# Kernel optimization log

Measured on AMD Instinct MI355X. Metric: run time of the kernel, lower is better.

Reference implementation:

```python
import jax, jax.numpy as jnp
import numpy as np

NUM_EXPERTS = 4


def _conv1x1(w, b, x):
    # w: [out,in], b: [out], x: [B,in,H,W]
    return jnp.einsum('oc,bchw->bohw', w, x) + b[None, :, None, None]


def _sobel(x):
    c = x.shape[1]
    kx = jnp.array([[-1., 0., 1.], [-2., 0., 2.], [-1., 0., 1.]], dtype=x.dtype)
    ky = jnp.array([[-1., -2., -1.], [0., 0., 0.], [1., 2., 1.]], dtype=x.dtype)
    wx = jnp.broadcast_to(kx[None, None], (c, 1, 3, 3))
    wy = jnp.broadcast_to(ky[None, None], (c, 1, 3, 3))
    dn = ('NCHW', 'OIHW', 'NCHW')
    gx = jax.lax.conv_general_dilated(x, wx, (1, 1), [(1, 1), (1, 1)],
                                      dimension_numbers=dn, feature_group_count=c)
    gy = jax.lax.conv_general_dilated(x, wy, (1, 1), [(1, 1), (1, 1)],
                                      dimension_numbers=dn, feature_group_count=c)
    return gx, gy


def _bilinear_sample(x, gx, gy):
    # torch F.grid_sample(mode='bilinear', padding_mode='zeros', align_corners=False)
    # x: [B,C,H,W]; gx, gy: [B,Hs,Ws] normalized coords in [-1,1]
    B, C, H, W = x.shape
    ix = ((gx + 1.0) * W - 1.0) * 0.5
    iy = ((gy + 1.0) * H - 1.0) * 0.5
    x0 = jnp.floor(ix)
    y0 = jnp.floor(iy)
    wx1 = ix - x0
    wx0 = 1.0 - wx1
    wy1 = iy - y0
    wy0 = 1.0 - wy1
    xf = x.reshape(B, C, H * W)

    def gather(xc, yc):
        valid = (xc >= 0) & (xc <= W - 1) & (yc >= 0) & (yc <= H - 1)
        xi = jnp.clip(xc, 0, W - 1).astype(jnp.int32)
        yi = jnp.clip(yc, 0, H - 1).astype(jnp.int32)
        idx = yi * W + xi  # [B,Hs,Ws]
        v = jax.vmap(lambda xb, ib: xb[:, ib])(xf, idx)  # [B,C,Hs,Ws]
        return v * valid[:, None].astype(x.dtype)

    return (gather(x0, y0) * (wx0 * wy0)[:, None]
            + gather(x0 + 1, y0) * (wx1 * wy0)[:, None]
            + gather(x0, y0 + 1) * (wx0 * wy1)[:, None]
            + gather(x0 + 1, y0 + 1) * (wx1 * wy1)[:, None])


def _forward(x, wc_e, we_e, wb1, bb1, wb2, bb2, wr, br, wo, bo, wcv, bcv, scale, scale2):
    B, c, h, w = x.shape
    sh = round(h * scale)
    sw = round(w * scale2)

    grad_x, grad_y = _sobel(x)

    # relative-offset coordinate embedding, [1,4,sh,sw]
    ih = (jnp.arange(sh, dtype=x.dtype) + 0.5) / scale
    coor_h = ih - jnp.floor(ih + 0.001) - 0.5  # [sh]
    iw = (jnp.arange(sw, dtype=x.dtype) + 0.5) / scale2
    coor_w = iw - jnp.floor(iw + 0.001) - 0.5  # [sw]
    inp = jnp.stack([
        jnp.full((sh, sw), 1.0 / scale2, dtype=x.dtype),
        jnp.full((sh, sw), 1.0 / scale, dtype=x.dtype),
        jnp.broadcast_to(coor_h[:, None], (sh, sw)),
        jnp.broadcast_to(coor_w[None, :], (sh, sw)),
    ], axis=0)[None]

    emb = jax.nn.relu(_conv1x1(wb2, bb2, jax.nn.relu(_conv1x1(wb1, bb1, inp))))
    offset = _conv1x1(wo, bo, emb)                 # [1,2,sh,sw]
    routing = jax.nn.sigmoid(_conv1x1(wr, br, emb))  # [1,E,sh,sw]

    # per-pixel soft mixture of expert compress/expand matrices
    rw = routing.reshape(NUM_EXPERTS, sh * sw).T   # [N,E]
    wc = (rw @ wc_e.reshape(NUM_EXPERTS, -1)).reshape(sh, sw, c // 8, c)
    we = (rw @ we_e.reshape(NUM_EXPERTS, -1)).reshape(sh, sw, c, c // 8)

    feat = _conv1x1(wcv, bcv, jnp.concatenate([x, grad_x, grad_y], axis=1))  # [B,64,h,w]

    # base grid (align_corners=True-style normalization, as in the source) + learned offsets
    gx0 = ((jnp.arange(sw, dtype=x.dtype) + 0.5) / scale2 - 0.5) * 2.0 / (w - 1) - 1.0
    gy0 = ((jnp.arange(sh, dtype=x.dtype) + 0.5) / scale - 0.5) * 2.0 / (h - 1) - 1.0
    gx = jnp.broadcast_to(gx0[None, None, :] + offset[:, 0] * (2.0 / (w - 1)), (B, sh, sw))
    gy = jnp.broadcast_to(gy0[None, :, None] + offset[:, 1] * (2.0 / (h - 1)), (B, sh, sw))

    fea0 = _bilinear_sample(feat, gx, gy)          # [B,64,sh,sw]

    mid = jnp.einsum('hwkc,bchw->bhwk', wc, fea0)  # per-pixel compress (k=C//8)
    out = jnp.einsum('hwck,bhwk->bchw', we, mid)   # per-pixel expand
    return out + fea0


def setup_inputs() -> dict:
    key = jax.random.key(0)
    ks = jax.random.split(key, 13)
    s = 0.05
    return {
        'x': jax.random.normal(ks[0], (2, 64, 192, 192), jnp.float32),
        'weight_compress': jax.random.normal(ks[1], (4, 8, 64), jnp.float32) * s,
        'weight_expand': jax.random.normal(ks[2], (4, 64, 8), jnp.float32) * s,
        'w_body1': jax.random.normal(ks[3], (64, 4), jnp.float32) * s,
        'b_body1': jax.random.normal(ks[4], (64,), jnp.float32) * s,
        'w_body2': jax.random.normal(ks[5], (64, 64), jnp.float32) * s,
        'b_body2': jax.random.normal(ks[6], (64,), jnp.float32) * s,
        'w_routing': jax.random.normal(ks[7], (4, 64), jnp.float32) * s,
        'b_routing': jax.random.normal(ks[8], (4,), jnp.float32) * s,
        'w_offset': jax.random.normal(ks[9], (2, 64), jnp.float32) * s,
        'b_offset': jax.random.normal(ks[10], (2,), jnp.float32) * s,
        'w_conv': jax.random.normal(ks[11], (64, 192), jnp.float32) * s,
        'b_conv': jax.random.normal(ks[12], (64,), jnp.float32) * s,
        'scale': 2,
        'scale2': 2,
    }


def reference(x, weight_compress, weight_expand, w_body1, b_body1, w_body2, b_body2,
              w_routing, b_routing, w_offset, b_offset, w_conv, b_conv, scale, scale2):
    return _forward(x, weight_compress, weight_expand, w_body1, b_body1, w_body2, b_body2,
                    w_routing, b_routing, w_offset, b_offset, w_conv, b_conv, scale, scale2)
```

## Files before the change

kernel.cpp:

```cpp
#include <hip/hip_runtime.h>
#include <hip/hip_bf16.h>
#include <math.h>

#define BN  2
#define CN  64
#define HN  192
#define WN  192
#define SH  384
#define SW  384
#define HW  (HN * WN)
#define NPIX (BN * HN * WN)

typedef __attribute__((ext_vector_type(8))) short bf16x8;
typedef __attribute__((ext_vector_type(4))) float f32x4;

#define KPAD 200

__device__ inline unsigned short f2bf(float f) {
    unsigned int u = __float_as_uint(f);
    u += 0x7fffu + ((u >> 16) & 1u);
    return (unsigned short)(u >> 16);
}

__device__ inline void sobel_col(const float* __restrict__ xc,
    size_t oT, size_t oM, size_t oB, int j, int jL, int jR,
    float mt, float mb, float mLt, float mLm, float mLb,
    float mRt, float mRm, float mRb, bool isL, bool isR,
    float& m_out, float& sx, float& sy)
{
    float t   = xc[oT + j] * mt;
    float m   = xc[oM + j];
    float btm = xc[oB + j] * mb;
    float hLt = xc[oT + jL] * mLt;
    float hLm = xc[oM + jL] * mLm;
    float hLb = xc[oB + jL] * mLb;
    float hRt = xc[oT + jR] * mRt;
    float hRm = xc[oM + jR] * mRm;
    float hRb = xc[oB + jR] * mRb;
    float tl  = __shfl_up(t, 1),   ml_ = __shfl_up(m, 1),   bl_ = __shfl_up(btm, 1);
    float tr  = __shfl_down(t, 1), mr_ = __shfl_down(m, 1), br_ = __shfl_down(btm, 1);
    float n0 = isL ? hLt : tl;
    float n3 = isL ? hLm : ml_;
    float n6 = isL ? hLb : bl_;
    float n2 = isR ? hRt : tr;
    float n5 = isR ? hRm : mr_;
    float n8 = isR ? hRb : br_;
    m_out = m;
    sx = (n2 - n0) + 2.f * (n5 - n3) + (n8 - n6);
    sy = (n6 - n0) + 2.f * (btm - t) + (n8 - n2);
}

__global__ __launch_bounds__(256) void feat_kernel(
    const float* __restrict__ x,
    const float* __restrict__ wcv,
    const float* __restrict__ bcv,
    float* __restrict__ feat)
{
    __shared__ unsigned short Bs[64 * KPAD];

    int bi = blockIdx.x;
    int jt = bi % 3;
    int t2 = bi / 3;
    int i  = t2 % HN;
    int b  = t2 / HN;
    int j0 = jt * 64;

    int tid  = threadIdx.x;
    int w    = __builtin_amdgcn_readfirstlane(tid >> 6);
    int lane = tid & 63;

    int mrow = (w << 4) + (lane & 15);
    int kb   = (lane >> 4) << 3;
    bf16x8 afrag[6];
    {
        const float* wr_ = wcv + mrow * 192 + kb;
#pragma unroll
        for (int ks = 0; ks < 6; ++ks) {
            float4 lo = *(const float4*)(wr_ + ks * 32);
            float4 hi = *(const float4*)(wr_ + ks * 32 + 4);
            bf16x8 a;
            a[0] = (short)f2bf(lo.x); a[1] = (short)f2bf(lo.y);
            a[2] = (short)f2bf(lo.z); a[3] = (short)f2bf(lo.w);
            a[4] = (short)f2bf(hi.x); a[5] = (short)f2bf(hi.y);
            a[6] = (short)f2bf(hi.z); a[7] = (short)f2bf(hi.w);
            afrag[ks] = a;
        }
    }

    bool ok_t = (i > 0), ok_b = (i < HN - 1);
    bool okL = (j0 > 0), okR = (j0 + 64 < WN);
    float mt = ok_t ? 1.f : 0.f, mb = ok_b ? 1.f : 0.f;
    int rT = ok_t ? i - 1 : i;
    int rB = ok_b ? i + 1 : i;
    int jL = okL ? j0 - 1 : j0;
    int jR = okR ? j0 + 64 : j0;
    float mLt = okL ? mt : 0.f, mLm = okL ? 1.f : 0.f, mLb = okL ? mb : 0.f;
    float mRt = okR ? mt : 0.f, mRm = okR ? 1.f : 0.f, mRb = okR ? mb : 0.f;
    bool isL = (lane == 0), isR = (lane == 63);

    const float* xb = x + (size_t)b * CN * HW;
    size_t oT = (size_t)rT * WN, oM = (size_t)i * WN, oB = (size_t)rB * WN;
    int j = j0 + lane;

    unsigned short* brow = Bs + lane * KPAD;
#pragma unroll 2
    for (int cp = 0; cp < 8; ++cp) {
        int c0 = (w << 4) + (cp << 1);
        float m0, sx0, sy0, m1, sx1, sy1;
        sobel_col(xb + (size_t)c0 * HW, oT, oM, oB, j, jL, jR,
                  mt, mb, mLt, mLm, mLb, mRt, mRm, mRb, isL, isR, m0, sx0, sy0);
        sobel_col(xb + (size_t)(c0 + 1) * HW, oT, oM, oB, j, jL, jR,
                  mt, mb, mLt, mLm, mLb, mRt, mRm, mRb, isL, isR, m1, sx1, sy1);
        *(unsigned int*)(brow + c0)       = (unsigned int)f2bf(m0)  | ((unsigned int)f2bf(m1)  << 16);
        *(unsigned int*)(brow + 64 + c0)  = (unsigned int)f2bf(sx0) | ((unsigned int)f2bf(sx1) << 16);
        *(unsigned int*)(brow + 128 + c0) = (unsigned int)f2bf(sy0) | ((unsigned int)f2bf(sy1) << 16);
    }

    __syncthreads();

    f32x4 acc[4] = {};
    const unsigned short* bp = Bs + (lane & 15) * KPAD + ((lane >> 4) << 3);
#pragma unroll
    for (int nt = 0; nt < 4; ++nt) {
        const unsigned short* bnt = bp + nt * 16 * KPAD;
#pragma unroll
        for (int ks = 0; ks < 6; ++ks) {
            bf16x8 bf = *(const bf16x8*)(bnt + ks * 32);
            acc[nt] = __builtin_amdgcn_mfma_f32_16x16x32_bf16(afrag[ks], bf, acc[nt], 0, 0, 0);
        }
    }

    int n0 = j0 + (lane & 15);
    int mbase = (w << 4) + ((lane >> 4) << 2);
    size_t outb = (size_t)b * CN * HW + (size_t)i * WN;
#pragma unroll
    for (int rr = 0; rr < 4; ++rr) {
        int m = mbase + rr;
        float bias = bcv[m];
        size_t rowb = outb + (size_t)m * HW + n0;
#pragma unroll
        for (int nt = 0; nt < 4; ++nt)
            feat[rowb + nt * 16] = acc[nt][rr] + bias;
    }
}

__device__ inline void run_mlp(int lane, float in0, float in1, float chv, float cwv,
    const float* __restrict__ wb1, const float* __restrict__ bb1,
    const float* __restrict__ wb2, const float* __restrict__ bb2,
    const float* __restrict__ wr,  const float* __restrict__ wo, float p[6])
{
    float4 w1 = ((const float4*)wb1)[lane];
    float h1 = fmaxf(bb1[lane] + w1.x * in0 + w1.y * in1 + w1.z * chv + w1.w * cwv, 0.f);
    const float4* w2row = (const float4*)(wb2 + lane * 64);
    float acc = bb2[lane];
#pragma unroll
    for (int q = 0; q < 16; ++q) {
        float4 wv = w2row[q];
        acc += wv.x * __shfl(h1, q * 4 + 0)
             + wv.y * __shfl(h1, q * 4 + 1)
             + wv.z * __shfl(h1, q * 4 + 2)
             + wv.w * __shfl(h1, q * 4 + 3);
    }
    float h2 = fmaxf(acc, 0.f);
#pragma unroll
    for (int e = 0; e < 4; ++e) p[e] = wr[e * 64 + lane] * h2;
#pragma unroll
    for (int e = 0; e < 2; ++e) p[4 + e] = wo[e * 64 + lane] * h2;
#pragma unroll
    for (int m = 1; m < 64; m <<= 1) {
#pragma unroll
        for (int e = 0; e < 6; ++e) p[e] += __shfl_xor(p[e], m);
    }
}

__global__ __launch_bounds__(256) void mlp_table_kernel(
    const float* __restrict__ wb1, const float* __restrict__ bb1,
    const float* __restrict__ wb2, const float* __restrict__ bb2,
    const float* __restrict__ wr,  const float* __restrict__ br,
    const float* __restrict__ wo,  const float* __restrict__ bo,
    const float* __restrict__ wce, const float* __restrict__ wee,
    const int* __restrict__ scale_p, const int* __restrict__ scale2_p,
    float* __restrict__ tblEntry, unsigned short* __restrict__ tblM)
{
    __shared__ float reL[8];
    __shared__ float wcmL[2 * 512];
    __shared__ float wemL[2 * 512];

    int sc = scale_p[0], sc2 = scale2_p[0];
    int tid = threadIdx.x;
    int lane = tid & 63;
    float scale = (float)sc, scale2 = (float)sc2;
    float in0 = 1.f / scale2, in1 = 1.f / scale;
    bool fast = (sc2 == 2 && sc <= 16);

    if (fast) {
        int pi = blockIdx.x;
        if (pi >= sc) return;
        if (tid < 64) {
            float ih = (pi + 0.5f) / scale;
            float chv = ih - floorf(ih + 0.001f) - 0.5f;
            float p0[6], p1[6];
            {
                float iw = 0.5f / scale2;
                float cwv = iw - floorf(iw + 0.001f) - 0.5f;
                run_mlp(lane, in0, in1, chv, cwv, wb1, bb1, wb2, bb2, wr, wo, p0);
            }
            {
                float iw = 1.5f / scale2;
                float cwv = iw - floorf(iw + 0.001f) - 0.5f;
                run_mlp(lane, in0, in1, chv, cwv, wb1, bb1, wb2, bb2, wr, wo, p1);
            }
            if (lane == 0) {
                float* t0 = tblEntry + (pi * 2 + 0) * 8;
                float* t1 = tblEntry + (pi * 2 + 1) * 8;
#pragma unroll
                for (int e = 0; e < 4; ++e) {
                    float rE = 1.f / (1.f + expf(-(p0[e] + br[e])));
                    float rO = 1.f / (1.f + expf(-(p1[e] + br[e])));
                    t0[e] = rE; t1[e] = rO;
                    reL[e] = rE; reL[4 + e] = rO;
                }
                t0[4] = p0[4] + bo[0]; t0[5] = p0[5] + bo[1];
                t1[4] = p1[4] + bo[0]; t1[5] = p1[5] + bo[1];
            }
        }
        __syncthreads();
        float reE0 = reL[0], reE1 = reL[1], reE2 = reL[2], reE3 = reL[3];
        float reO0 = reL[4], reO1 = reL[5], reO2 = reL[6], reO3 = reL[7];
        for (int idx = tid; idx < 512; idx += 256) {
            float a = wce[idx], bq = wce[512 + idx], c = wce[1024 + idx], d = wce[1536 + idx];
            wcmL[idx]       = reE0 * a + reE1 * bq + reE2 * c + reE3 * d;
            wcmL[512 + idx] = reO0 * a + reO1 * bq + reO2 * c + reO3 * d;
            float e_ = wee[idx], f = wee[512 + idx], g = wee[1024 + idx], h = wee[1536 + idx];
            wemL[idx]       = reE0 * e_ + reE1 * f + reE2 * g + reE3 * h;
            wemL[512 + idx] = reO0 * e_ + reO1 * f + reO2 * g + reO3 * h;
        }
        __syncthreads();
        int co  = tid >> 2;
        int ci0 = (tid & 3) << 4;
        float w0[8], w1[8];
#pragma unroll
        for (int k = 0; k < 8; ++k) {
            w0[k] = wemL[co * 8 + k];
            w1[k] = wemL[512 + co * 8 + k];
        }
        unsigned short* tb = tblM + (size_t)pi * 2 * 4096;
#pragma unroll
        for (int cc = 0; cc < 16; ++cc) {
            int ci = ci0 + cc;
            float m0 = 0.f, m1 = 0.f;
#pragma unroll
            for (int k = 0; k < 8; ++k) {
                m0 += w0[k] * wcmL[k * 64 + ci];
                m1 += w1[k] * wcmL[512 + k * 64 + ci];
            }
            tb[co * 64 + ci]        = f2bf(0.5f * (m0 + m1));
            tb[4096 + co * 64 + ci] = f2bf(0.5f * (m0 - m1));
        }
    } else {
        int w = (blockIdx.x * 256 + threadIdx.x) >> 6;
        if (w >= sc * sc2) return;
        int pi = w / sc2, pj = w - pi * sc2;
        float ih = (pi + 0.5f) / scale;
        float chv = ih - floorf(ih + 0.001f) - 0.5f;
        float iw = (pj + 0.5f) / scale2;
        float cwv = iw - floorf(iw + 0.001f) - 0.5f;
        float p[6];
        run_mlp(lane, in0, in1, chv, cwv, wb1, bb1, wb2, bb2, wr, wo, p);
        if (lane == 0) {
            float* tp = tblEntry + w * 8;
#pragma unroll
            for (int e = 0; e < 4; ++e) tp[e] = 1.f / (1.f + expf(-(p[e] + br[e])));
            tp[4] = p[4] + bo[0];
            tp[5] = p[5] + bo[1];
        }
    }
}

#define BKP 72
__global__ __launch_bounds__(256) void out_kernel(
    const float* __restrict__ feat,
    const float* __restrict__ tblEntry,
    const unsigned short* __restrict__ tblM,
    const float* __restrict__ wce,
    const float* __restrict__ wee,
    const int* __restrict__ scale_p, const int* __restrict__ scale2_p,
    float* __restrict__ out)
{
    __shared__ __attribute__((aligned(16))) float smem[64 * 65 + 64 * (BKP / 2)];
    float* fea32 = smem;
    unsigned short* Bsv = (unsigned short*)(smem + 64 * 65);
    float* midp = smem;

    int Bk = blockIdx.x;
    int T = gridDim.x;
    int t = ((T & 7) == 0) ? ((Bk & 7) * (T >> 3) + (Bk >> 3)) : Bk;

    int tid = threadIdx.x;
    int g = __builtin_amdgcn_readfirstlane(tid >> 6);
    int lane = tid & 63;
    int pix0 = t * 64;
    int b = pix0 / (SH * SW);
    int r0 = pix0 - b * SH * SW;
    int i = r0 / SW;
    int j0 = r0 - i * SW;
    int j = j0 + lane;
    int r = r0 + lane;

    int sc = scale_p[0], sc2 = scale2_p[0];
    float scale = (float)sc, scale2 = (float)sc2;
    int pi = i - (i / sc) * sc;
    int pj = j - (j / sc2) * sc2;
    int entry = pi * sc2 + pj;
    float offx = tblEntry[entry * 8 + 4];
    float offy = tblEntry[entry * 8 + 5];

    const float inv_wm1 = 2.f / (float)(WN - 1);
    const float inv_hm1 = 2.f / (float)(HN - 1);
    float gx = ((j + 0.5f) / scale2 - 0.5f) * inv_wm1 - 1.f + offx * inv_wm1;
    float gy = ((i + 0.5f) / scale  - 0.5f) * inv_hm1 - 1.f + offy * inv_hm1;

    float ix = ((gx + 1.f) * WN - 1.f) * 0.5f;
    float iy = ((gy + 1.f) * HN - 1.f) * 0.5f;
    float fx0 = floorf(ix), fy0 = floorf(iy);
    int x0 = (int)fx0, y0 = (int)fy0;
    float wx1 = ix - fx0, wx0 = 1.f - wx1;
    float wy1 = iy - fy0, wy0 = 1.f - wy1;

    bool vx0 = (x0 >= 0) && (x0 <= WN - 1);
    bool vx1 = (x0 + 1 >= 0) && (x0 + 1 <= WN - 1);
    bool vy0 = (y0 >= 0) && (y0 <= HN - 1);
    bool vy1 = (y0 + 1 >= 0) && (y0 + 1 <= HN - 1);
    bool v00 = vx0 && vy0, v10 = vx1 && vy0, v01 = vx0 && vy1, v11 = vx1 && vy1;
    float w00 = wx0 * wy0, w10 = wx1 * wy0, w01 = wx0 * wy1, w11 = wx1 * wy1;

    int i00 = y0 * WN + x0;
    int i10 = i00 + 1;
    int i01 = i00 + WN;
    int i11 = i01 + 1;

    const float* fb = feat + (size_t)b * CN * HW;

    float f0[16];
#pragma unroll
    for (int cc = 0; cc < 16; ++cc) {
        const float* fc = fb + (size_t)(g * 16 + cc) * HW;
        float a  = v00 ? fc[i00] : 0.f;
        float bq = v10 ? fc[i10] : 0.f;
        float cq = v01 ? fc[i01] : 0.f;
        float dq = v11 ? fc[i11] : 0.f;
        f0[cc] = a * w00 + bq * w10 + cq * w01 + dq * w11;
    }

    bool fast = (sc2 == 2 && sc <= 16);
    if (fast) {
        int px = lane;
#pragma unroll
        for (int cc = 0; cc < 16; ++cc)
            fea32[px * 65 + g * 16 + cc] = f0[cc];
#pragma unroll
        for (int cc = 0; cc < 16; cc += 2) {
            unsigned int pk = (unsigned int)f2bf(f0[cc]) | ((unsigned int)f2bf(f0[cc + 1]) << 16);
            *(unsigned int*)(Bsv + px * BKP + g * 16 + cc) = pk;
        }

        int row = lane & 15;
        int kb  = (lane >> 4) << 3;
        const unsigned short* Mb = tblM + (size_t)pi * 2 * 4096 + (g * 16 + row) * 64 + kb;
        bf16x8 a1[2], a2[2];
        a1[0] = *(const bf16x8*)(Mb);
        a1[1] = *(const bf16x8*)(Mb + 32);
        a2[0] = *(const bf16x8*)(Mb + 4096);
        a2[1] = *(const bf16x8*)(Mb + 4096 + 32);

        __syncthreads();

        f32x4 acc1[4] = {}, acc2[4] = {};
        const unsigned short* bp = Bsv + (lane & 15) * BKP + kb;
#pragma unroll
        for (int nt = 0; nt < 4; ++nt) {
            const unsigned short* bnt = bp + nt * 16 * BKP;
#pragma unroll
            for (int ks = 0; ks < 2; ++ks) {
                bf16x8 bf = *(const bf16x8*)(bnt + ks * 32);
                acc1[nt] = __builtin_amdgcn_mfma_f32_16x16x32_bf16(a1[ks], bf, acc1[nt], 0, 0, 0);
                acc2[nt] = __builtin_amdgcn_mfma_f32_16x16x32_bf16(a2[ks], bf, acc2[nt], 0, 0, 0);
            }
        }

        int q = lane >> 4;
#pragma unroll
        for (int rr = 0; rr < 4; ++rr) {
            int c = g * 16 + q * 4 + rr;
            size_t rowb = (size_t)(b * CN + c) * SH * SW + r0;
#pragma unroll
            for (int nt = 0; nt < 4; ++nt) {
                int n = (lane & 15) + nt * 16;
                float sgn = (n & 1) ? -1.f : 1.f;
                float v = fea32[n * 65 + c] + acc1[nt][rr] + sgn * acc2[nt][rr];
                out[rowb + n] = v;
            }
        }
    } else {
        float4 rw = *(const float4*)(tblEntry + entry * 8);
        float re[4] = {rw.x, rw.y, rw.z, rw.w};
        float part[4][8];
#pragma unroll
        for (int e = 0; e < 4; ++e) {
#pragma unroll
            for (int k = 0; k < 8; ++k) {
                const float* wrow = wce + (e * 8 + k) * 64 + g * 16;
                float d = 0.f;
#pragma unroll
                for (int cc = 0; cc < 16; ++cc) d += wrow[cc] * f0[cc];
                part[e][k] = d;
            }
        }
#pragma unroll
        for (int k = 0; k < 8; ++k) {
            float m = re[0] * part[0][k] + re[1] * part[1][k]
                    + re[2] * part[2][k] + re[3] * part[3][k];
            midp[(g * 64 + lane) * 9 + k] = m;
        }
        __syncthreads();
        float mid[8];
#pragma unroll
        for (int k = 0; k < 8; ++k)
            mid[k] = midp[(0 * 64 + lane) * 9 + k] + midp[(1 * 64 + lane) * 9 + k]
                   + midp[(2 * 64 + lane) * 9 + k] + midp[(3 * 64 + lane) * 9 + k];
#pragma unroll
        for (int cc = 0; cc < 16; ++cc) {
            int c = g * 16 + cc;
            float v = f0[cc];
#pragma unroll
            for (int e = 0; e < 4; ++e) {
                const float* wrow = wee + (e * 64 + c) * 8;
                float d = 0.f;
#pragma unroll
                for (int k = 0; k < 8; ++k) d += wrow[k] * mid[k];
                v += re[e] * d;
            }
            out[(size_t)(b * CN + c) * SH * SW + r] = v;
        }
    }
}

extern "C" void kernel_launch(void* const* d_in, const int* in_sizes, int n_in,
                              void* d_out, int out_size, void* d_ws, size_t ws_size,
                              hipStream_t stream) {
    const float* x    = (const float*)d_in[0];
    const float* wce  = (const float*)d_in[1];
    const float* wee  = (const float*)d_in[2];
    const float* wb1  = (const float*)d_in[3];
    const float* bb1  = (const float*)d_in[4];
    const float* wb2  = (const float*)d_in[5];
    const float* bb2  = (const float*)d_in[6];
    const float* wr   = (const float*)d_in[7];
    const float* br   = (const float*)d_in[8];
    const float* wo   = (const float*)d_in[9];
    const float* bo   = (const float*)d_in[10];
    const float* wcv  = (const float*)d_in[11];
    const float* bcv  = (const float*)d_in[12];
    const int*   scale  = (const int*)d_in[13];
    const int*   scale2 = (const int*)d_in[14];
    float* out = (float*)d_out;

    float* feat     = (float*)d_ws;
    float* tblEntry = feat + (size_t)BN * CN * HW;
    unsigned short* tblM = (unsigned short*)(tblEntry + 256 * 8);

    feat_kernel<<<BN * HN * 3, 256, 0, stream>>>(x, wcv, bcv, feat);
    mlp_table_kernel<<<64, 256, 0, stream>>>(wb1, bb1, wb2, bb2, wr, br, wo, bo,
                                             wce, wee, scale, scale2,
                                             tblEntry, tblM);
    out_kernel<<<BN * SH * SW / 64, 256, 0, stream>>>(feat, tblEntry, tblM,
                                                      wce, wee, scale, scale2, out);
}
```

Baseline: 162.2 us.

## Fold Sobel into 3x3 conv weights and merge feature and table kernels

Folds the Sobel filters and the 1x1 conv into nine per-tap bf16 weight matrices, so the feature map is computed as a 3x3 convolution by MFMA over a bf16 halo tile of x held in shared memory. Each block now handles two output rows, and the MLP table computation runs in extra blocks of the same launch, which removes one kernel launch. This triples the MFMA work per output and adds register pressure from 18 weight fragments. In exchange it removes the per-channel Sobel shuffles and the redundant halo loads, and x is now rounded to bf16 before the stencil rather than after.

New measurement: 150.6 us. -7.1%, faster.

```diff
diff --git a/kernel.cpp b/kernel.cpp
--- a/kernel.cpp
+++ b/kernel.cpp
@@ -14,134 +14,18 @@
 typedef __attribute__((ext_vector_type(8))) short bf16x8;
 typedef __attribute__((ext_vector_type(4))) float f32x4;
 
-#define KPAD 200
+#define ROWS  2
+#define CPAD  72
+#define MAINB (BN * (HN / ROWS) * 3)
+#define TBLB  64
 
 __device__ inline unsigned short f2bf(float f) {
     unsigned int u = __float_as_uint(f);
     u += 0x7fffu + ((u >> 16) & 1u);
     return (unsigned short)(u >> 16);
 }
-
-__device__ inline void sobel_col(const float* __restrict__ xc,
-    size_t oT, size_t oM, size_t oB, int j, int jL, int jR,
-    float mt, float mb, float mLt, float mLm, float mLb,
-    float mRt, float mRm, float mRb, bool isL, bool isR,
-    float& m_out, float& sx, float& sy)
-{
-    float t   = xc[oT + j] * mt;
-    float m   = xc[oM + j];
-    float btm = xc[oB + j] * mb;
-    float hLt = xc[oT + jL] * mLt;
-    float hLm = xc[oM + jL] * mLm;
-    float hLb = xc[oB + jL] * mLb;
-    float hRt = xc[oT + jR] * mRt;
-    float hRm = xc[oM + jR] * mRm;
-    float hRb = xc[oB + jR] * mRb;
-    float tl  = __shfl_up(t, 1),   ml_ = __shfl_up(m, 1),   bl_ = __shfl_up(btm, 1);
-    float tr  = __shfl_down(t, 1), mr_ = __shfl_down(m, 1), br_ = __shfl_down(btm, 1);
-    float n0 = isL ? hLt : tl;
-    float n3 = isL ? hLm : ml_;
-    float n6 = isL ? hLb : bl_;
-    float n2 = isR ? hRt : tr;
-    float n5 = isR ? hRm : mr_;
-    float n8 = isR ? hRb : br_;
-    m_out = m;
-    sx = (n2 - n0) + 2.f * (n5 - n3) + (n8 - n6);
-    sy = (n6 - n0) + 2.f * (btm - t) + (n8 - n2);
-}
-
-__global__ __launch_bounds__(256) void feat_kernel(
-    const float* __restrict__ x,
-    const float* __restrict__ wcv,
-    const float* __restrict__ bcv,
-    float* __restrict__ feat)
-{
-    __shared__ unsigned short Bs[64 * KPAD];
-
-    int bi = blockIdx.x;
-    int jt = bi % 3;
-    int t2 = bi / 3;
-    int i  = t2 % HN;
-    int b  = t2 / HN;
-    int j0 = jt * 64;
-
-    int tid  = threadIdx.x;
-    int w    = __builtin_amdgcn_readfirstlane(tid >> 6);
-    int lane = tid & 63;
-
-    int mrow = (w << 4) + (lane & 15);
-    int kb   = (lane >> 4) << 3;
-    bf16x8 afrag[6];
-    {
-        const float* wr_ = wcv + mrow * 192 + kb;
-#pragma unroll
-        for (int ks = 0; ks < 6; ++ks) {
-            float4 lo = *(const float4*)(wr_ + ks * 32);
-            float4 hi = *(const float4*)(wr_ + ks * 32 + 4);
-            bf16x8 a;
-            a[0] = (short)f2bf(lo.x); a[1] = (short)f2bf(lo.y);
-            a[2] = (short)f2bf(lo.z); a[3] = (short)f2bf(lo.w);
-            a[4] = (short)f2bf(hi.x); a[5] = (short)f2bf(hi.y);
-            a[6] = (short)f2bf(hi.z); a[7] = (short)f2bf(hi.w);
-            afrag[ks] = a;
-        }
-    }
-
-    bool ok_t = (i > 0), ok_b = (i < HN - 1);
-    bool okL = (j0 > 0), okR = (j0 + 64 < WN);
-    float mt = ok_t ? 1.f : 0.f, mb = ok_b ? 1.f : 0.f;
-    int rT = ok_t ? i - 1 : i;
-    int rB = ok_b ? i + 1 : i;
-    int jL = okL ? j0 - 1 : j0;
-    int jR = okR ? j0 + 64 : j0;
-    float mLt = okL ? mt : 0.f, mLm = okL ? 1.f : 0.f, mLb = okL ? mb : 0.f;
-    float mRt = okR ? mt : 0.f, mRm = okR ? 1.f : 0.f, mRb = okR ? mb : 0.f;
-    bool isL = (lane == 0), isR = (lane == 63);
-
-    const float* xb = x + (size_t)b * CN * HW;
-    size_t oT = (size_t)rT * WN, oM = (size_t)i * WN, oB = (size_t)rB * WN;
-    int j = j0 + lane;
-
-    unsigned short* brow = Bs + lane * KPAD;
-#pragma unroll 2
-    for (int cp = 0; cp < 8; ++cp) {
-        int c0 = (w << 4) + (cp << 1);
-        float m0, sx0, sy0, m1, sx1, sy1;
-        sobel_col(xb + (size_t)c0 * HW, oT, oM, oB, j, jL, jR,
-                  mt, mb, mLt, mLm, mLb, mRt, mRm, mRb, isL, isR, m0, sx0, sy0);
-        sobel_col(xb + (size_t)(c0 + 1) * HW, oT, oM, oB, j, jL, jR,
-                  mt, mb, mLt, mLm, mLb, mRt, mRm, mRb, isL, isR, m1, sx1, sy1);
-        *(unsigned int*)(brow + c0)       = (unsigned int)f2bf(m0)  | ((unsigned int)f2bf(m1)  << 16);
-        *(unsigned int*)(brow + 64 + c0)  = (unsigned int)f2bf(sx0) | ((unsigned int)f2bf(sx1) << 16);
-        *(unsigned int*)(brow + 128 + c0) = (unsigned int)f2bf(sy0) | ((unsigned int)f2bf(sy1) << 16);
-    }
-
-    __syncthreads();
-
-    f32x4 acc[4] = {};
-    const unsigned short* bp = Bs + (lane & 15) * KPAD + ((lane >> 4) << 3);
-#pragma unroll
-    for (int nt = 0; nt < 4; ++nt) {
-        const unsigned short* bnt = bp + nt * 16 * KPAD;
-#pragma unroll
-        for (int ks = 0; ks < 6; ++ks) {
-            bf16x8 bf = *(const bf16x8*)(bnt + ks * 32);
-            acc[nt] = __builtin_amdgcn_mfma_f32_16x16x32_bf16(afrag[ks], bf, acc[nt], 0, 0, 0);
-        }
-    }
-
-    int n0 = j0 + (lane & 15);
-    int mbase = (w << 4) + ((lane >> 4) << 2);
-    size_t outb = (size_t)b * CN * HW + (size_t)i * WN;
-#pragma unroll
-    for (int rr = 0; rr < 4; ++rr) {
-        int m = mbase + rr;
-        float bias = bcv[m];
-        size_t rowb = outb + (size_t)m * HW + n0;
-#pragma unroll
-        for (int nt = 0; nt < 4; ++nt)
-            feat[rowb + nt * 16] = acc[nt][rr] + bias;
-    }
+__device__ inline unsigned int pkbf(float a, float b) {
+    return (unsigned int)f2bf(a) | ((unsigned int)f2bf(b) << 16);
 }
 
 __device__ inline void run_mlp(int lane, float in0, float in1, float chv, float cwv,
@@ -173,7 +57,11 @@
     }
 }
 
-__global__ __launch_bounds__(256) void mlp_table_kernel(
+__global__ __launch_bounds__(256) void feat_table_kernel(
+    const float* __restrict__ x,
+    const float* __restrict__ wcv,
+    const float* __restrict__ bcv,
+    float* __restrict__ feat,
     const float* __restrict__ wb1, const float* __restrict__ bb1,
     const float* __restrict__ wb2, const float* __restrict__ bb2,
     const float* __restrict__ wr,  const float* __restrict__ br,
@@ -182,97 +70,231 @@
     const int* __restrict__ scale_p, const int* __restrict__ scale2_p,
     float* __restrict__ tblEntry, unsigned short* __restrict__ tblM)
 {
-    __shared__ float reL[8];
-    __shared__ float wcmL[2 * 512];
-    __shared__ float wemL[2 * 512];
-
-    int sc = scale_p[0], sc2 = scale2_p[0];
-    int tid = threadIdx.x;
+    __shared__ __attribute__((aligned(16))) unsigned short smem_u16[4 * 66 * CPAD];
+
+    int tid  = threadIdx.x;
     int lane = tid & 63;
-    float scale = (float)sc, scale2 = (float)sc2;
-    float in0 = 1.f / scale2, in1 = 1.f / scale;
-    bool fast = (sc2 == 2 && sc <= 16);
-
-    if (fast) {
-        int pi = blockIdx.x;
-        if (pi >= sc) return;
-        if (tid < 64) {
+
+    if (blockIdx.x >= MAINB) {
+        float* wcmL = (float*)smem_u16;
+        float* wemL = wcmL + 1024;
+        float* reL  = wemL + 1024;
+
+        int sc = scale_p[0], sc2 = scale2_p[0];
+        float scale = (float)sc, scale2 = (float)sc2;
+        float in0 = 1.f / scale2, in1 = 1.f / scale;
+        bool fast = (sc2 == 2 && sc <= 16);
+        int tb = blockIdx.x - MAINB;
+
+        if (fast) {
+            int pi = tb;
+            if (pi >= sc) return;
+            if (tid < 64) {
+                float ih = (pi + 0.5f) / scale;
+                float chv = ih - floorf(ih + 0.001f) - 0.5f;
+                float p0[6], p1[6];
+                {
+                    float iw = 0.5f / scale2;
+                    float cwv = iw - floorf(iw + 0.001f) - 0.5f;
+                    run_mlp(lane, in0, in1, chv, cwv, wb1, bb1, wb2, bb2, wr, wo, p0);
+                }
+                {
+                    float iw = 1.5f / scale2;
+                    float cwv = iw - floorf(iw + 0.001f) - 0.5f;
+                    run_mlp(lane, in0, in1, chv, cwv, wb1, bb1, wb2, bb2, wr, wo, p1);
+                }
+                if (lane == 0) {
+                    float* t0 = tblEntry + (pi * 2 + 0) * 8;
+                    float* t1 = tblEntry + (pi * 2 + 1) * 8;
+#pragma unroll
+                    for (int e = 0; e < 4; ++e) {
+                        float rE = 1.f / (1.f + expf(-(p0[e] + br[e])));
+                        float rO = 1.f / (1.f + expf(-(p1[e] + br[e])));
+                        t0[e] = rE; t1[e] = rO;
+                        reL[e] = rE; reL[4 + e] = rO;
+                    }
+                    t0[4] = p0[4] + bo[0]; t0[5] = p0[5] + bo[1];
+                    t1[4] = p1[4] + bo[0]; t1[5] = p1[5] + bo[1];
+                }
+            }
+            __syncthreads();
+            float reE0 = reL[0], reE1 = reL[1], reE2 = reL[2], reE3 = reL[3];
+            float reO0 = reL[4], reO1 = reL[5], reO2 = reL[6], reO3 = reL[7];
+            for (int idx = tid; idx < 512; idx += 256) {
+                float a = wce[idx], bq = wce[512 + idx], c = wce[1024 + idx], d = wce[1536 + idx];
+                wcmL[idx]       = reE0 * a + reE1 * bq + reE2 * c + reE3 * d;
+                wcmL[512 + idx] = reO0 * a + reO1 * bq + reO2 * c + reO3 * d;
+                float e_ = wee[idx], f = wee[512 + idx], g = wee[1024 + idx], h = wee[1536 + idx];
+                wemL[idx]       = reE0 * e_ + reE1 * f + reE2 * g + reE3 * h;
+                wemL[512 + idx] = reO0 * e_ + reO1 * f + reO2 * g + reO3 * h;
+            }
+            __syncthreads();
+            int co  = tid >> 2;
+            int ci0 = (tid & 3) << 4;
+            float w0[8], w1[8];
+#pragma unroll
+            for (int k = 0; k < 8; ++k) {
+                w0[k] = wemL[co * 8 + k];
+                w1[k] = wemL[512 + co * 8 + k];
+            }
+            unsigned short* tbp = tblM + (size_t)pi * 2 * 4096;
+#pragma unroll
+            for (int cc = 0; cc < 16; ++cc) {
+                int ci = ci0 + cc;
+                float m0 = 0.f, m1 = 0.f;
+#pragma unroll
+                for (int k = 0; k < 8; ++k) {
+                    m0 += w0[k] * wcmL[k * 64 + ci];
+                    m1 += w1[k] * wcmL[512 + k * 64 + ci];
+                }
+                tbp[co * 64 + ci]        = f2bf(0.5f * (m0 + m1));
+                tbp[4096 + co * 64 + ci] = f2bf(0.5f * (m0 - m1));
+            }
+        } else {
+            int w_ = (tb * 256 + tid) >> 6;
+            if (w_ >= sc * sc2) return;
+            int pi = w_ / sc2, pj = w_ - pi * sc2;
             float ih = (pi + 0.5f) / scale;
             float chv = ih - floorf(ih + 0.001f) - 0.5f;
-            float p0[6], p1[6];
-            {
-                float iw = 0.5f / scale2;
-                float cwv = iw - floorf(iw + 0.001f) - 0.5f;
-                run_mlp(lane, in0, in1, chv, cwv, wb1, bb1, wb2, bb2, wr, wo, p0);
-            }
-            {
-                float iw = 1.5f / scale2;
-                float cwv = iw - floorf(iw + 0.001f) - 0.5f;
-                run_mlp(lane, in0, in1, chv, cwv, wb1, bb1, wb2, bb2, wr, wo, p1);
-            }
+            float iw = (pj + 0.5f) / scale2;
+            float cwv = iw - floorf(iw + 0.001f) - 0.5f;
+            float p[6];
+            run_mlp(lane, in0, in1, chv, cwv, wb1, bb1, wb2, bb2, wr, wo, p);
             if (lane == 0) {
-                float* t0 = tblEntry + (pi * 2 + 0) * 8;
-                float* t1 = tblEntry + (pi * 2 + 1) * 8;
-#pragma unroll
-                for (int e = 0; e < 4; ++e) {
-                    float rE = 1.f / (1.f + expf(-(p0[e] + br[e])));
-                    float rO = 1.f / (1.f + expf(-(p1[e] + br[e])));
-                    t0[e] = rE; t1[e] = rO;
-                    reL[e] = rE; reL[4 + e] = rO;
-                }
-                t0[4] = p0[4] + bo[0]; t0[5] = p0[5] + bo[1];
-                t1[4] = p1[4] + bo[0]; t1[5] = p1[5] + bo[1];
-            }
-        }
-        __syncthreads();
-        float reE0 = reL[0], reE1 = reL[1], reE2 = reL[2], reE3 = reL[3];
-        float reO0 = reL[4], reO1 = reL[5], reO2 = reL[6], reO3 = reL[7];
-        for (int idx = tid; idx < 512; idx += 256) {
-            float a = wce[idx], bq = wce[512 + idx], c = wce[1024 + idx], d = wce[1536 + idx];
-            wcmL[idx]       = reE0 * a + reE1 * bq + reE2 * c + reE3 * d;
-            wcmL[512 + idx] = reO0 * a + reO1 * bq + reO2 * c + reO3 * d;
-            float e_ = wee[idx], f = wee[512 + idx], g = wee[1024 + idx], h = wee[1536 + idx];
-            wemL[idx]       = reE0 * e_ + reE1 * f + reE2 * g + reE3 * h;
-            wemL[512 + idx] = reO0 * e_ + reO1 * f + reO2 * g + reO3 * h;
-        }
-        __syncthreads();
-        int co  = tid >> 2;
-        int ci0 = (tid & 3) << 4;
-        float w0[8], w1[8];
-#pragma unroll
-        for (int k = 0; k < 8; ++k) {
-            w0[k] = wemL[co * 8 + k];
-            w1[k] = wemL[512 + co * 8 + k];
-        }
-        unsigned short* tb = tblM + (size_t)pi * 2 * 4096;
-#pragma unroll
-        for (int cc = 0; cc < 16; ++cc) {
-            int ci = ci0 + cc;
-            float m0 = 0.f, m1 = 0.f;
-#pragma unroll
-            for (int k = 0; k < 8; ++k) {
-                m0 += w0[k] * wcmL[k * 64 + ci];
-                m1 += w1[k] * wcmL[512 + k * 64 + ci];
-            }
-            tb[co * 64 + ci]        = f2bf(0.5f * (m0 + m1));
-            tb[4096 + co * 64 + ci] = f2bf(0.5f * (m0 - m1));
-        }
-    } else {
-        int w = (blockIdx.x * 256 + threadIdx.x) >> 6;
-        if (w >= sc * sc2) return;
-        int pi = w / sc2, pj = w - pi * sc2;
-        float ih = (pi + 0.5f) / scale;
-        float chv = ih - floorf(ih + 0.001f) - 0.5f;
-        float iw = (pj + 0.5f) / scale2;
-        float cwv = iw - floorf(iw + 0.001f) - 0.5f;
-        float p[6];
-        run_mlp(lane, in0, in1, chv, cwv, wb1, bb1, wb2, bb2, wr, wo, p);
-        if (lane == 0) {
-            float* tp = tblEntry + w * 8;
-#pragma unroll
-            for (int e = 0; e < 4; ++e) tp[e] = 1.f / (1.f + expf(-(p[e] + br[e])));
-            tp[4] = p[4] + bo[0];
-            tp[5] = p[5] + bo[1];
+                float* tp = tblEntry + w_ * 8;
+#pragma unroll
+                for (int e = 0; e < 4; ++e) tp[e] = 1.f / (1.f + expf(-(p[e] + br[e])));
+                tp[4] = p[4] + bo[0];
+                tp[5] = p[5] + bo[1];
+            }
+        }
+        return;
+    }
+
+    int bi = blockIdx.x;
+    int jt = bi % 3;
+    int t2 = bi / 3;
+    int it = t2 % (HN / ROWS);
+    int b  = t2 / (HN / ROWS);
+    int i0 = it * ROWS;
+    int j0 = jt * 64;
+    int w  = __builtin_amdgcn_readfirstlane(tid >> 6);
+
+    int row = lane & 15;
+    int q   = lane >> 4;
+
+    const float KXc[9] = {-1.f, 0.f, 1.f, -2.f, 0.f, 2.f, -1.f, 0.f, 1.f};
+    const float KYc[9] = {-1.f, -2.f, -1.f, 0.f, 0.f, 0.f, 1.f, 2.f, 1.f};
+    bf16x8 afrag[9][2];
+    {
+        int o = (w << 4) + row;
+        const float* wp = wcv + o * 192;
+        float v0[2][8], v1[2][8], v2[2][8];
+#pragma unroll
+        for (int kc = 0; kc < 2; ++kc) {
+            int kb = kc * 32 + q * 8;
+            float4 a0 = *(const float4*)(wp + kb);
+            float4 a1 = *(const float4*)(wp + kb + 4);
+            float4 b0 = *(const float4*)(wp + 64 + kb);
+            float4 b1 = *(const float4*)(wp + 64 + kb + 4);
+            float4 c0 = *(const float4*)(wp + 128 + kb);
+            float4 c1 = *(const float4*)(wp + 128 + kb + 4);
+            v0[kc][0]=a0.x; v0[kc][1]=a0.y; v0[kc][2]=a0.z; v0[kc][3]=a0.w;
+            v0[kc][4]=a1.x; v0[kc][5]=a1.y; v0[kc][6]=a1.z; v0[kc][7]=a1.w;
+            v1[kc][0]=b0.x; v1[kc][1]=b0.y; v1[kc][2]=b0.z; v1[kc][3]=b0.w;
+            v1[kc][4]=b1.x; v1[kc][5]=b1.y; v1[kc][6]=b1.z; v1[kc][7]=b1.w;
+            v2[kc][0]=c0.x; v2[kc][1]=c0.y; v2[kc][2]=c0.z; v2[kc][3]=c0.w;
+            v2[kc][4]=c1.x; v2[kc][5]=c1.y; v2[kc][6]=c1.z; v2[kc][7]=c1.w;
+        }
+#pragma unroll
+        for (int t = 0; t < 9; ++t) {
+#pragma unroll
+            for (int kc = 0; kc < 2; ++kc) {
+                bf16x8 a;
+#pragma unroll
+                for (int e = 0; e < 8; ++e) {
+                    float f = v1[kc][e] * KXc[t] + v2[kc][e] * KYc[t];
+                    if (t == 4) f += v0[kc][e];
+                    a[e] = (short)f2bf(f);
+                }
+                afrag[t][kc] = a;
+            }
+        }
+    }
+
+    {
+        int sr = i0 - 1 + w;
+        bool rok = (sr >= 0) && (sr < HN);
+        int src = rok ? sr : 0;
+        int hc = j0 - 1 + lane;
+        bool cok = (hc >= 0) && (hc < WN);
+        int hcc = cok ? hc : 0;
+        float msk = (rok && cok) ? 1.f : 0.f;
+        const float* p = x + (size_t)b * CN * HW + (size_t)src * WN + hcc;
+        unsigned short* xrow = smem_u16 + (w * 66 + lane) * CPAD;
+#pragma unroll 4
+        for (int k = 0; k < 16; ++k) {
+            int c0 = k << 2;
+            float a0 = p[0] * msk;
+            float a1 = p[(size_t)HW] * msk;
+            float a2 = p[2 * (size_t)HW] * msk;
+            float a3 = p[3 * (size_t)HW] * msk;
+            uint2 uu;
+            uu.x = pkbf(a0, a1);
+            uu.y = pkbf(a2, a3);
+            *(uint2*)(xrow + c0) = uu;
+            p += 4 * (size_t)HW;
+        }
+        if (lane < 32) {
+            int colx = 64 + (lane & 1);
+            int c0 = (lane >> 1) << 2;
+            int hx = j0 - 1 + colx;
+            bool cokx = (hx < WN);
+            int hxc = cokx ? hx : 0;
+            float mskx = (rok && cokx) ? 1.f : 0.f;
+            const float* px = x + ((size_t)b * CN + c0) * HW + (size_t)src * WN + hxc;
+            float a0 = px[0] * mskx;
+            float a1 = px[(size_t)HW] * mskx;
+            float a2 = px[2 * (size_t)HW] * mskx;
+            float a3 = px[3 * (size_t)HW] * mskx;
+            uint2 uu;
+            uu.x = pkbf(a0, a1);
+            uu.y = pkbf(a2, a3);
+            *(uint2*)(smem_u16 + (w * 66 + colx) * CPAD + c0) = uu;
+        }
+    }
+
+    __syncthreads();
+
+    f32x4 acc[2][4] = {};
+    const unsigned short* bb0 = smem_u16 + row * CPAD + (q << 3);
+#pragma unroll
+    for (int ro = 0; ro < 2; ++ro) {
+#pragma unroll
+        for (int nt = 0; nt < 4; ++nt) {
+#pragma unroll
+            for (int t = 0; t < 9; ++t) {
+                int a_ = t / 3, dxi = t - a_ * 3;
+#pragma unroll
+                for (int kc = 0; kc < 2; ++kc) {
+                    bf16x8 bv = *(const bf16x8*)(bb0 + ((ro + a_) * 66 + nt * 16 + dxi) * CPAD + kc * 32);
+                    acc[ro][nt] = __builtin_amdgcn_mfma_f32_16x16x32_bf16(afrag[t][kc], bv, acc[ro][nt], 0, 0, 0);
+                }
+            }
+        }
+    }
+
+#pragma unroll
+    for (int ro = 0; ro < 2; ++ro) {
+        size_t rb0 = (size_t)b * CN * HW + (size_t)(i0 + ro) * WN + j0 + row;
+#pragma unroll
+        for (int rr = 0; rr < 4; ++rr) {
+            int oc = (w << 4) + q * 4 + rr;
+            float bias = bcv[oc];
+            size_t rowb = rb0 + (size_t)oc * HW;
+#pragma unroll
+            for (int nt = 0; nt < 4; ++nt)
+                feat[rowb + nt * 16] = acc[ro][nt][rr] + bias;
         }
     }
 }
@@ -469,10 +491,9 @@
     float* tblEntry = feat + (size_t)BN * CN * HW;
     unsigned short* tblM = (unsigned short*)(tblEntry + 256 * 8);
 
-    feat_kernel<<<BN * HN * 3, 256, 0, stream>>>(x, wcv, bcv, feat);
-    mlp_table_kernel<<<64, 256, 0, stream>>>(wb1, bb1, wb2, bb2, wr, br, wo, bo,
-                                             wce, wee, scale, scale2,
-                                             tblEntry, tblM);
+    feat_table_kernel<<<MAINB + TBLB, 256, 0, stream>>>(
+        x, wcv, bcv, feat, wb1, bb1, wb2, bb2, wr, br, wo, bo,
+        wce, wee, scale, scale2, tblEntry, tblM);
     out_kernel<<<BN * SH * SW / 64, 256, 0, stream>>>(feat, tblEntry, tblM,
                                                       wce, wee, scale, scale2, out);
 }
```
